# Kernel tuning notes

Hardware: AMD Instinct MI355X
Metric: run time of the kernel (lower is better)

Reference implementation:

```python
import jax, jax.numpy as jnp
import numpy as np

B, C, H, W = 4, 256, 64, 64
G, K, PAD, STRIDE, DIL, DWK = 8, 3, 1, 1, 1, 3
P = K * K
GC = C // G


def _dwconv(x, w, b, pad):
    # x: (B,C,H,W), w: (C,1,k,k) depthwise
    y = jax.lax.conv_general_dilated(x, w, (1, 1), [(pad, pad), (pad, pad)],
                                     feature_group_count=C,
                                     dimension_numbers=('NCHW', 'OIHW', 'NCHW'))
    return y + b[None, :, None, None]


def _conv1x1(x, w, b):
    # x: (B,Cin,H,W), w: (Cin,Cout)
    return jnp.einsum('bchw,cd->bdhw', x, w) + b[None, :, None, None]


def _ln(x, g, b, eps=1e-5):
    mu = x.mean(-1, keepdims=True)
    var = ((x - mu) ** 2).mean(-1, keepdims=True)
    return (x - mu) * jax.lax.rsqrt(var + eps) * g + b


def _bilinear_sample(img, grid):
    # img: (GC, Hp, Wp); grid: (L, P, 2) in [-1,1]; F.grid_sample bilinear,
    # padding_mode='zeros', align_corners=False
    gc, Hp, Wp = img.shape
    ix = ((grid[..., 0] + 1.0) * Wp - 1.0) * 0.5
    iy = ((grid[..., 1] + 1.0) * Hp - 1.0) * 0.5
    x0 = jnp.floor(ix); y0 = jnp.floor(iy)
    x1 = x0 + 1.0;      y1 = y0 + 1.0
    imgf = img.reshape(gc, Hp * Wp)

    def gather(yy, xx):
        valid = (xx >= 0) & (xx <= Wp - 1) & (yy >= 0) & (yy <= Hp - 1)
        xi = jnp.clip(xx, 0, Wp - 1).astype(jnp.int32)
        yi = jnp.clip(yy, 0, Hp - 1).astype(jnp.int32)
        return imgf[:, yi * Wp + xi] * valid  # (GC, L, P)

    w00 = (x1 - ix) * (y1 - iy); w01 = (ix - x0) * (y1 - iy)
    w10 = (x1 - ix) * (iy - y0); w11 = (ix - x0) * (iy - y0)
    return (gather(y0, x0) * w00 + gather(y0, x1) * w01 +
            gather(y1, x0) * w10 + gather(y1, x1) * w11)


def _dcnv3_core(x, offset, mask):
    # x: (B,H,W,C); offset: (B,H,W,G*P*2); mask: (B,H,W,G*P) softmaxed over P
    xp = jnp.pad(x, ((0, 0), (PAD, PAD), (PAD, PAD), (0, 0)))
    Hp, Wp = H + 2 * PAD, W + 2 * PAD
    base = (DIL * (K - 1)) // 2 + 0.5
    ref_y = (base + jnp.arange(H, dtype=jnp.float32) * STRIDE) / Hp
    ref_x = (base + jnp.arange(W, dtype=jnp.float32) * STRIDE) / Wp
    ref = jnp.stack([jnp.broadcast_to(ref_x[None, :], (H, W)),
                     jnp.broadcast_to(ref_y[:, None], (H, W))], -1)  # (H,W,2) (x,y)
    lin = jnp.arange(K, dtype=jnp.float32) * DIL - (DIL * (K - 1)) // 2
    gx, gy = jnp.meshgrid(lin, lin, indexing='ij')  # x-outer (torch meshgrid order)
    dil_grid = jnp.stack([gx / Wp, gy / Hp], -1).reshape(P, 2)
    loc = ref[:, :, None, None, :] + dil_grid[None, None, None, :, :]  # (H,W,1,P,2)
    loc = jnp.broadcast_to(loc, (H, W, G, P, 2))[None]
    norm = jnp.array([Wp, Hp], jnp.float32)
    loc = loc + offset.reshape(B, H, W, G, P, 2) / norm  # offset_scale=1.0
    sg = 2.0 * loc - 1.0  # (B,H,W,G,P,2)
    xin = xp.reshape(B, Hp, Wp, G, GC).transpose(0, 3, 4, 1, 2).reshape(B * G, GC, Hp, Wp)
    sgf = sg.reshape(B, H * W, G, P, 2).transpose(0, 2, 1, 3, 4).reshape(B * G, H * W, P, 2)
    sampled = jax.vmap(_bilinear_sample)(xin, sgf)  # (B*G, GC, HW, P)
    m = mask.reshape(B, H * W, G, P).transpose(0, 2, 1, 3).reshape(B * G, 1, H * W, P)
    out = (sampled * m).sum(-1)  # (B*G, GC, HW)
    return out.reshape(B, G, GC, H * W).transpose(0, 3, 1, 2).reshape(B, H, W, C)


def _dcn(x, inproj_w, inproj_b, dw_w, dw_b, ln_g, ln_b,
         off_w, off_b, mask_w, mask_b, outproj_w, outproj_b):
    # x: (B,H,W,C) -> DCNv3_pytorch forward
    xproj = x @ inproj_w + inproj_b
    x1 = _dwconv(x.transpose(0, 3, 1, 2), dw_w, dw_b, (DWK - 1) // 2).transpose(0, 2, 3, 1)
    x1 = jax.nn.gelu(_ln(x1, ln_g, ln_b), approximate=False)
    offset = x1 @ off_w + off_b
    m = jax.nn.softmax((x1 @ mask_w + mask_b).reshape(B, H, W, G, P), -1).reshape(B, H, W, G * P)
    out = _dcnv3_core(xproj, offset, m)
    return out @ outproj_w + outproj_b


def _forward(x, proj1_w, proj1_b, conv0_w, conv0_b, inproj_w, inproj_b,
             dw_w, dw_b, ln_g, ln_b, off_w, off_b, mask_w, mask_b,
             outproj_w, outproj_b, conv_w, conv_b, proj2_w, proj2_b):
    shortcut = x
    h = jax.nn.gelu(_conv1x1(x, proj1_w, proj1_b), approximate=False)
    u = h
    h = _dwconv(h, conv0_w, conv0_b, 2)  # 5x5 depthwise, pad 2
    attn = _dcn(h.transpose(0, 2, 3, 1), inproj_w, inproj_b, dw_w, dw_b,
                ln_g, ln_b, off_w, off_b, mask_w, mask_b, outproj_w, outproj_b)
    attn = _conv1x1(attn.transpose(0, 3, 1, 2), conv_w, conv_b)
    h = _conv1x1(u * attn, proj2_w, proj2_b)
    return h + shortcut


def setup_inputs():
    key = jax.random.key(0)
    ks = jax.random.split(key, 12)
    s = lambda k, shape, fan: jax.random.normal(k, shape, jnp.float32) / np.sqrt(fan)
    return {
        'x': jax.random.normal(ks[0], (B, C, H, W), jnp.float32),
        'proj1_w': s(ks[1], (C, C), C), 'proj1_b': jnp.zeros((C,), jnp.float32),
        'conv0_w': s(ks[2], (C, 1, 5, 5), 25), 'conv0_b': jnp.zeros((C,), jnp.float32),
        'inproj_w': s(ks[3], (C, C), C), 'inproj_b': jnp.zeros((C,), jnp.float32),
        'dw_w': s(ks[4], (C, 1, DWK, DWK), DWK * DWK), 'dw_b': jnp.zeros((C,), jnp.float32),
        'ln_g': jnp.ones((C,), jnp.float32), 'ln_b': jnp.zeros((C,), jnp.float32),
        'off_w': s(ks[5], (C, G * P * 2), C) * 0.1, 'off_b': jnp.zeros((G * P * 2,), jnp.float32),
        'mask_w': s(ks[6], (C, G * P), C), 'mask_b': jnp.zeros((G * P,), jnp.float32),
        'outproj_w': s(ks[7], (C, C), C), 'outproj_b': jnp.zeros((C,), jnp.float32),
        'conv_w': s(ks[8], (C, C), C), 'conv_b': jnp.zeros((C,), jnp.float32),
        'proj2_w': s(ks[9], (C, C), C), 'proj2_b': jnp.zeros((C,), jnp.float32),
    }


def reference(x, proj1_w, proj1_b, conv0_w, conv0_b, inproj_w, inproj_b,
              dw_w, dw_b, ln_g, ln_b, off_w, off_b, mask_w, mask_b,
              outproj_w, outproj_b, conv_w, conv_b, proj2_w, proj2_b):
    return _forward(x, proj1_w, proj1_b, conv0_w, conv0_b, inproj_w, inproj_b,
                    dw_w, dw_b, ln_g, ln_b, off_w, off_b, mask_w, mask_b,
                    outproj_w, outproj_b, conv_w, conv_b, proj2_w, proj2_b)
```

## Files before the change

kernel.cpp:

```cpp
#include <hip/hip_runtime.h>
#include <cstddef>

#define HW    4096
#define NPIX  16384
#define CCH   256

typedef __attribute__((ext_vector_type(8))) short bf16x8;
typedef __attribute__((ext_vector_type(4))) float f32x4;

__device__ __forceinline__ float gelu_f(float x){
    return 0.5f * x * (1.0f + erff(x * 0.70710678118654752f));
}

__device__ __forceinline__ unsigned short bf_rne(float f){
    unsigned u = __float_as_uint(f);
    u += 0x7FFFu + ((u >> 16) & 1u);
    return (unsigned short)(u >> 16);
}

__device__ __forceinline__ void split_cheap(const float4 a, const float4 b, bf16x8& hi, bf16x8& lo){
    const float v[8] = {a.x,a.y,a.z,a.w,b.x,b.y,b.z,b.w};
    #pragma unroll
    for (int j = 0; j < 8; j++){
        const unsigned u = __float_as_uint(v[j]);
        hi[j] = (short)(unsigned short)(u >> 16);
        const float r = v[j] - __uint_as_float(u & 0xFFFF0000u);
        lo[j] = (short)(unsigned short)(__float_as_uint(r) >> 16);
    }
}

__global__ __launch_bounds__(256) void k_prep(const float* __restrict__ w5,
                                              const float* __restrict__ w3,
                                              float* __restrict__ wT,
                                              float* __restrict__ wT3){
    const int c = threadIdx.x;
    const int j = blockIdx.x;
    wT[j * CCH + c] = w5[c * 25 + j];
    if (j < 9) wT3[j * CCH + c] = w3[c * 9 + j];
}

__global__ __launch_bounds__(256) void k_compose(const float* __restrict__ ow,
                                                 const float* __restrict__ cw,
                                                 const float* __restrict__ ob,
                                                 const float* __restrict__ cb,
                                                 float* __restrict__ woc,
                                                 float* __restrict__ boc){
    const int m = threadIdx.x;
    if (blockIdx.x == 256){
        float acc = cb[m];
        #pragma unroll 4
        for (int k = 0; k < 256; k++) acc = fmaf(ob[k], cw[k * 256 + m], acc);
        boc[m] = acc;
    } else {
        const int r = blockIdx.x;
        const float* orow = ow + r * 256;
        float acc = 0.f;
        #pragma unroll 4
        for (int k = 0; k < 256; k++) acc = fmaf(orow[k], cw[k * 256 + m], acc);
        woc[r * 256 + m] = acc;
    }
}

__global__ __launch_bounds__(256) void k_prep_w(
    const float* __restrict__ w0, const float* __restrict__ w1, const float* __restrict__ w2,
    const float* __restrict__ w3,
    const float* __restrict__ offw, const float* __restrict__ maskw,
    const float* __restrict__ offb, const float* __restrict__ maskb,
    unsigned short* __restrict__ wsp, float* __restrict__ bcat)
{
    __shared__ float tile[64][65];
    const int id = blockIdx.y;
    const int m0 = (blockIdx.x & 3) * 64;
    const int k0 = (blockIdx.x >> 2) * 64;
    const int tx = threadIdx.x & 63, tg = threadIdx.x >> 6;
    unsigned short* hi = wsp + (size_t)id * 131072;
    unsigned short* lo = hi + 65536;

    const int m = m0 + tx;
    const float* src = nullptr; int stride = 0; bool valid = true;
    if (id == 4){
        if (m < 144){ src = offw + m; stride = 144; }
        else if (m < 216){ src = maskw + (m - 144); stride = 72; }
        else valid = false;
    } else {
        const float* s = (id==0)?w0:(id==1)?w1:(id==2)?w2:w3;
        src = s + m; stride = 256;
    }
    #pragma unroll
    for (int i = 0; i < 16; i++){
        const int kl = tg * 16 + i;
        tile[kl][tx] = valid ? src[(size_t)(k0 + kl) * stride] : 0.f;
    }
    __syncthreads();
    #pragma unroll
    for (int i = 0; i < 16; i++){
        const int ml = tg * 16 + i;
        const float f = tile[tx][ml];
        const unsigned u = __float_as_uint(f);
        const size_t o = (size_t)(m0 + ml) * 256 + k0 + tx;
        hi[o] = (unsigned short)(u >> 16);
        lo[o] = bf_rne(f - __uint_as_float(u & 0xFFFF0000u));
    }
    if (id == 4 && blockIdx.x == 0){
        const int t = threadIdx.x;
        if (t < 216) bcat[t] = (t < 144) ? offb[t] : maskb[t - 144];
        else if (t < 224) bcat[t] = 0.f;
    }
}

__global__ __launch_bounds__(256) void k_transpose(const float* __restrict__ in,
                                                   float* __restrict__ out){
    __shared__ float tile[64][65];
    const int b = blockIdx.z, c0 = blockIdx.y * 64, hw0 = blockIdx.x * 64;
    const int tx = threadIdx.x & 63, tg = threadIdx.x >> 6;
    #pragma unroll
    for (int i = 0; i < 16; i++){
        const int c_l = tg * 16 + i;
        tile[c_l][tx] = in[(size_t)(b * CCH + c0 + c_l) * HW + hw0 + tx];
    }
    __syncthreads();
    #pragma unroll
    for (int i = 0; i < 16; i++){
        const int hw_l = tg * 16 + i;
        out[(size_t)(b * HW + hw0 + hw_l) * CCH + c0 + tx] = tile[tx][hw_l];
    }
}

template<int EPI, bool MUL>
__global__ __launch_bounds__(256) void k_gemm_bf(
    const float* __restrict__ A, const float* __restrict__ A2,
    const unsigned short* __restrict__ Whi, const unsigned short* __restrict__ Wlo,
    const float* __restrict__ bias, const float* __restrict__ resid,
    float* __restrict__ out, const int M, const int ldc)
{
    const int rows0 = blockIdx.x * 32;
    const int lane = threadIdx.x & 63;
    const int w    = threadIdx.x >> 6;
    const int wm = (w >> 1) * 16;
    const int wn = (w & 1) * 128;
    const int lr = lane & 15;
    const int kg = lane >> 4;
    const int kl = kg * 8;

    const float* Ap = A + (size_t)(rows0 + wm + lr) * 256 + kl;
    const float* Mp = MUL ? (A2 + (size_t)(rows0 + wm + lr) * 256 + kl) : nullptr;
    const int c0 = wn + lr;
    const unsigned short* Wh = Whi + (size_t)c0 * 256 + kl;
    const unsigned short* Wl = Wlo + (size_t)c0 * 256 + kl;

    const f32x4 z = {0.f, 0.f, 0.f, 0.f};
    f32x4 acc[8] = {z,z,z,z,z,z,z,z};

    #pragma unroll 2
    for (int kt = 0; kt < 8; kt++){
        const int k0 = kt * 32;
        float4 a0 = *reinterpret_cast<const float4*>(Ap + k0);
        float4 a1 = *reinterpret_cast<const float4*>(Ap + k0 + 4);
        if (MUL){
            const float4 u0 = *reinterpret_cast<const float4*>(Mp + k0);
            const float4 u1 = *reinterpret_cast<const float4*>(Mp + k0 + 4);
            a0.x*=u0.x; a0.y*=u0.y; a0.z*=u0.z; a0.w*=u0.w;
            a1.x*=u1.x; a1.y*=u1.y; a1.z*=u1.z; a1.w*=u1.w;
        }
        bf16x8 ah, al;
        split_cheap(a0, a1, ah, al);
        #pragma unroll
        for (int nf = 0; nf < 8; nf++){
            const size_t wo = (size_t)(nf * 16) * 256 + k0;
            const bf16x8 bh = *reinterpret_cast<const bf16x8*>(Wh + wo);
            const bf16x8 bl = *reinterpret_cast<const bf16x8*>(Wl + wo);
            acc[nf] = __builtin_amdgcn_mfma_f32_16x16x32_bf16(ah, bh, acc[nf], 0, 0, 0);
            acc[nf] = __builtin_amdgcn_mfma_f32_16x16x32_bf16(ah, bl, acc[nf], 0, 0, 0);
            acc[nf] = __builtin_amdgcn_mfma_f32_16x16x32_bf16(al, bh, acc[nf], 0, 0, 0);
        }
    }

    const int r4 = kg * 4;
    const int rowb = rows0 + wm + r4;
    if (EPI == 2){
        const int bimg = rowb >> 12;
        const int hw   = rowb & (HW - 1);
        #pragma unroll
        for (int nf = 0; nf < 8; nf++){
            const int col = c0 + nf * 16;
            const float bs = bias[col];
            const size_t addr = ((size_t)(bimg * CCH + col)) * HW + hw;
            const float4 rv = *reinterpret_cast<const float4*>(resid + addr);
            float4 o;
            o.x = acc[nf][0] + bs + rv.x;
            o.y = acc[nf][1] + bs + rv.y;
            o.z = acc[nf][2] + bs + rv.z;
            o.w = acc[nf][3] + bs + rv.w;
            *reinterpret_cast<float4*>(out + addr) = o;
        }
    } else {
        #pragma unroll
        for (int nf = 0; nf < 8; nf++){
            const int col = c0 + nf * 16;
            if (col < M){
                const float bs = bias[col];
                #pragma unroll
                for (int r = 0; r < 4; r++){
                    float v = acc[nf][r] + bs;
                    if (EPI == 1) v = gelu_f(v);
                    out[(size_t)(rowb + r) * ldc + col] = v;
                }
            }
        }
    }
}

__global__ __launch_bounds__(256) void k_dwconv5(const float* __restrict__ in,
                                                 const float* __restrict__ wT,
                                                 const float* __restrict__ bias,
                                                 float* __restrict__ out){
    const int lane = threadIdx.x & 63;
    const int pq   = threadIdx.x >> 6;
    const int n = blockIdx.x * 4 + pq;
    const int x = n & 63, y = (n >> 6) & 63, b = n >> 12;
    const int c = lane * 4;
    const float* bp = in + (size_t)(b * HW) * CCH + c;
    float4 acc = *reinterpret_cast<const float4*>(bias + c);
    #pragma unroll
    for (int k = 0; k < 25; k++){
        const int dy = k / 5 - 2, dx = k % 5 - 2;
        const int yy = y + dy, xx = x + dx;
        const float m = (((unsigned)yy < 64u) & ((unsigned)xx < 64u)) ? 1.f : 0.f;
        const int yc = min(max(yy, 0), 63), xc = min(max(xx, 0), 63);
        const float4 iv = *reinterpret_cast<const float4*>(bp + (size_t)(yc * 64 + xc) * CCH);
        const float4 wv = *reinterpret_cast<const float4*>(wT + k * CCH + c);
        acc.x = fmaf(iv.x, wv.x * m, acc.x);
        acc.y = fmaf(iv.y, wv.y * m, acc.y);
        acc.z = fmaf(iv.z, wv.z * m, acc.z);
        acc.w = fmaf(iv.w, wv.w * m, acc.w);
    }
    *reinterpret_cast<float4*>(out + (size_t)n * CCH + c) = acc;
}

__global__ __launch_bounds__(256) void k_dw3_ln_gelu(const float* __restrict__ in,
                                                     const float* __restrict__ wT3,
                                                     const float* __restrict__ b3,
                                                     const float* __restrict__ g,
                                                     const float* __restrict__ bta,
                                                     float* __restrict__ out){
    const int lane = threadIdx.x & 63;
    const int pq   = threadIdx.x >> 6;
    const int n = blockIdx.x * 4 + pq;
    const int x = n & 63, y = (n >> 6) & 63, b = n >> 12;
    const int c = lane * 4;
    const float* bp = in + (size_t)(b * HW) * CCH + c;
    float4 acc = *reinterpret_cast<const float4*>(b3 + c);
    #pragma unroll
    for (int k = 0; k < 9; k++){
        const int dy = k / 3 - 1, dx = k % 3 - 1;
        const int yy = y + dy, xx = x + dx;
        const float m = (((unsigned)yy < 64u) & ((unsigned)xx < 64u)) ? 1.f : 0.f;
        const int yc = min(max(yy, 0), 63), xc = min(max(xx, 0), 63);
        const float4 iv = *reinterpret_cast<const float4*>(bp + (size_t)(yc * 64 + xc) * CCH);
        const float4 wv = *reinterpret_cast<const float4*>(wT3 + k * CCH + c);
        acc.x = fmaf(iv.x, wv.x * m, acc.x);
        acc.y = fmaf(iv.y, wv.y * m, acc.y);
        acc.z = fmaf(iv.z, wv.z * m, acc.z);
        acc.w = fmaf(iv.w, wv.w * m, acc.w);
    }
    float s  = acc.x + acc.y + acc.z + acc.w;
    float s2 = acc.x*acc.x + acc.y*acc.y + acc.z*acc.z + acc.w*acc.w;
    #pragma unroll
    for (int o = 32; o > 0; o >>= 1){
        s  += __shfl_xor(s, o);
        s2 += __shfl_xor(s2, o);
    }
    const float mu  = s  * (1.f / 256.f);
    const float var = s2 * (1.f / 256.f) - mu * mu;
    const float r   = rsqrtf(var + 1e-5f);
    const float4 gv = *reinterpret_cast<const float4*>(g + c);
    const float4 bv = *reinterpret_cast<const float4*>(bta + c);
    float4 o;
    o.x = gelu_f((acc.x - mu) * r * gv.x + bv.x);
    o.y = gelu_f((acc.y - mu) * r * gv.y + bv.y);
    o.z = gelu_f((acc.z - mu) * r * gv.z + bv.z);
    o.w = gelu_f((acc.w - mu) * r * gv.w + bv.w);
    *reinterpret_cast<float4*>(out + (size_t)n * CCH + c) = o;
}

__global__ __launch_bounds__(256) void k_dcn(const float* __restrict__ xproj,
                                             const float* __restrict__ om,
                                             float* __restrict__ out){
    const int lane = threadIdx.x & 63;
    const int pq   = threadIdx.x >> 6;
    const int n = blockIdx.x * 4 + pq;
    const int gI = lane >> 3, cq = lane & 7;
    const int x = n & 63, y = (n >> 6) & 63, b = n >> 12;
    const float* off = om + (size_t)n * 216 + gI * 18;
    const float* lg  = om + (size_t)n * 216 + 144 + gI * 9;
    float l[9]; float mx = -1e30f;
    #pragma unroll
    for (int p = 0; p < 9; p++){ l[p] = lg[p]; mx = fmaxf(mx, l[p]); }
    float ssum = 0.f;
    #pragma unroll
    for (int p = 0; p < 9; p++){ l[p] = expf(l[p] - mx); ssum += l[p]; }
    const float inv = 1.f / ssum;
    const float* base = xproj + (size_t)b * HW * CCH + gI * 32 + cq * 4;
    float4 acc = {0.f, 0.f, 0.f, 0.f};
    #pragma unroll
    for (int p = 0; p < 9; p++){
        const float2 o2 = *reinterpret_cast<const float2*>(off + p * 2);
        const float ix = (float)(x + p / 3) + o2.x;
        const float iy = (float)(y + p % 3) + o2.y;
        const float x0f = floorf(ix), y0f = floorf(iy);
        const float wx1 = ix - x0f, wy1 = iy - y0f;
        const float wx0 = 1.f - wx1, wy0 = 1.f - wy1;
        const int ux = (int)x0f - 1, uy = (int)y0f - 1;
        const bool X0 = (unsigned)ux     < 64u, X1 = (unsigned)(ux+1) < 64u;
        const bool Y0 = (unsigned)uy     < 64u, Y1 = (unsigned)(uy+1) < 64u;
        const int ux0 = min(max(ux,     0), 63), ux1 = min(max(ux + 1, 0), 63);
        const int uy0 = min(max(uy,     0), 63), uy1 = min(max(uy + 1, 0), 63);
        const float mp = l[p] * inv;
        const float w00 = wx0 * wy0 * ((X0 & Y0) ? mp : 0.f);
        const float w01 = wx1 * wy0 * ((X1 & Y0) ? mp : 0.f);
        const float w10 = wx0 * wy1 * ((X0 & Y1) ? mp : 0.f);
        const float w11 = wx1 * wy1 * ((X1 & Y1) ? mp : 0.f);
        const float4 v00 = *reinterpret_cast<const float4*>(base + (size_t)(uy0 * 64 + ux0) * CCH);
        const float4 v01 = *reinterpret_cast<const float4*>(base + (size_t)(uy0 * 64 + ux1) * CCH);
        const float4 v10 = *reinterpret_cast<const float4*>(base + (size_t)(uy1 * 64 + ux0) * CCH);
        const float4 v11 = *reinterpret_cast<const float4*>(base + (size_t)(uy1 * 64 + ux1) * CCH);
        acc.x = fmaf(w00, v00.x, fmaf(w01, v01.x, fmaf(w10, v10.x, fmaf(w11, v11.x, acc.x))));
        acc.y = fmaf(w00, v00.y, fmaf(w01, v01.y, fmaf(w10, v10.y, fmaf(w11, v11.y, acc.y))));
        acc.z = fmaf(w00, v00.z, fmaf(w01, v01.z, fmaf(w10, v10.z, fmaf(w11, v11.z, acc.z))));
        acc.w = fmaf(w00, v00.w, fmaf(w01, v01.w, fmaf(w10, v10.w, fmaf(w11, v11.w, acc.w))));
    }
    *reinterpret_cast<float4*>(out + (size_t)n * CCH + gI * 32 + cq * 4) = acc;
}

extern "C" void kernel_launch(void* const* d_in, const int* in_sizes, int n_in,
                              void* d_out, int out_size, void* d_ws, size_t ws_size,
                              hipStream_t stream){
    const float* x         = (const float*)d_in[0];
    const float* proj1_w   = (const float*)d_in[1];
    const float* proj1_b   = (const float*)d_in[2];
    const float* conv0_w   = (const float*)d_in[3];
    const float* conv0_b   = (const float*)d_in[4];
    const float* inproj_w  = (const float*)d_in[5];
    const float* inproj_b  = (const float*)d_in[6];
    const float* dw_w      = (const float*)d_in[7];
    const float* dw_b      = (const float*)d_in[8];
    const float* ln_g      = (const float*)d_in[9];
    const float* ln_b      = (const float*)d_in[10];
    const float* off_w     = (const float*)d_in[11];
    const float* off_b     = (const float*)d_in[12];
    const float* mask_w    = (const float*)d_in[13];
    const float* mask_b    = (const float*)d_in[14];
    const float* outproj_w = (const float*)d_in[15];
    const float* outproj_b = (const float*)d_in[16];
    const float* conv_w    = (const float*)d_in[17];
    const float* conv_b    = (const float*)d_in[18];
    const float* proj2_w   = (const float*)d_in[19];
    const float* proj2_b   = (const float*)d_in[20];
    float* outp = (float*)d_out;

    const size_t NC = (size_t)NPIX * CCH;
    float* b0 = (float*)d_ws;
    float* b1 = b0 + NC;
    float* b2 = b1 + NC;
    float* b3 = outp;
    unsigned short* wsp = (unsigned short*)(b2 + NC);
    float* bcat = (float*)(wsp + 5 * 131072);
    float* woc  = bcat + 224;
    float* boc  = woc + 65536;
    float* wT   = b3;
    float* wT3  = b3 + 25 * CCH;

    const unsigned short* whi[5]; const unsigned short* wlo[5];
    for (int i = 0; i < 5; i++){ whi[i] = wsp + (size_t)i * 131072; wlo[i] = whi[i] + 65536; }

    k_prep<<<25,256,0,stream>>>(conv0_w, dw_w, wT, wT3);
    k_compose<<<257,256,0,stream>>>(outproj_w, conv_w, outproj_b, conv_b, woc, boc);
    k_prep_w<<<dim3(16,5),256,0,stream>>>(proj1_w, inproj_w, woc, proj2_w,
                                          off_w, mask_w, off_b, mask_b, wsp, bcat);
    k_transpose<<<dim3(64,4,4),256,0,stream>>>(x, b0);
    k_gemm_bf<1,false><<<512,256,0,stream>>>(b0, nullptr, whi[0], wlo[0], proj1_b, nullptr, b1, 256, 256);
    k_dwconv5<<<4096,256,0,stream>>>(b1, wT, conv0_b, b2);
    k_dw3_ln_gelu<<<4096,256,0,stream>>>(b2, wT3, dw_b, ln_g, ln_b, b0);
    k_gemm_bf<0,false><<<512,256,0,stream>>>(b2, nullptr, whi[1], wlo[1], inproj_b, nullptr, b3, 256, 256);
    k_gemm_bf<0,false><<<512,256,0,stream>>>(b0, nullptr, whi[4], wlo[4], bcat, nullptr, b2, 216, 216);
    k_dcn<<<4096,256,0,stream>>>(b3, b2, b0);
    k_gemm_bf<0,false><<<512,256,0,stream>>>(b0, nullptr, whi[2], wlo[2], boc, nullptr, b2, 256, 256);
    k_gemm_bf<2,true><<<512,256,0,stream>>>(b1, b2, whi[3], wlo[3], proj2_b, x, outp, 256, 256);
}
```

Baseline: 391.5 us.

## Retile bf16x3 GEMM to 64x128 blocks with 2D grid and vectorized epilogue

Changes the split-bf16 GEMM tiling from 32 rows by 256 columns per block to 64 rows by 128 columns, using a 2D grid so each wave computes a 32x64 tile that reuses each weight fragment across two row fragments. For the non-residual epilogues, MFMA operands are swapped so each lane holds four consecutive output columns, which allows float4 bias loads and float4 stores instead of scalar strided stores. The low-part split now uses round-to-nearest instead of truncation, trading a few extra ALU ops for accuracy.

```diff
diff --git a/kernel.cpp b/kernel.cpp
--- a/kernel.cpp
+++ b/kernel.cpp
@@ -18,14 +18,13 @@
     return (unsigned short)(u >> 16);
 }
 
-__device__ __forceinline__ void split_cheap(const float4 a, const float4 b, bf16x8& hi, bf16x8& lo){
+__device__ __forceinline__ void split2(const float4 a, const float4 b, bf16x8& hi, bf16x8& lo){
     const float v[8] = {a.x,a.y,a.z,a.w,b.x,b.y,b.z,b.w};
     #pragma unroll
     for (int j = 0; j < 8; j++){
         const unsigned u = __float_as_uint(v[j]);
         hi[j] = (short)(unsigned short)(u >> 16);
-        const float r = v[j] - __uint_as_float(u & 0xFFFF0000u);
-        lo[j] = (short)(unsigned short)(__float_as_uint(r) >> 16);
+        lo[j] = (short)bf_rne(v[j] - __uint_as_float(u & 0xFFFF0000u));
     }
 }
 
@@ -133,77 +132,106 @@
     const float* __restrict__ bias, const float* __restrict__ resid,
     float* __restrict__ out, const int M, const int ldc)
 {
-    const int rows0 = blockIdx.x * 32;
+    const int rows0 = blockIdx.x * 64;
+    const int cols0 = blockIdx.y * 128;
     const int lane = threadIdx.x & 63;
     const int w    = threadIdx.x >> 6;
-    const int wm = (w >> 1) * 16;
-    const int wn = (w & 1) * 128;
+    const int wm = (w >> 1) * 32, wn = (w & 1) * 64;
     const int lr = lane & 15;
     const int kg = lane >> 4;
     const int kl = kg * 8;
 
-    const float* Ap = A + (size_t)(rows0 + wm + lr) * 256 + kl;
-    const float* Mp = MUL ? (A2 + (size_t)(rows0 + wm + lr) * 256 + kl) : nullptr;
-    const int c0 = wn + lr;
-    const unsigned short* Wh = Whi + (size_t)c0 * 256 + kl;
-    const unsigned short* Wl = Wlo + (size_t)c0 * 256 + kl;
+    const float* Ap0 = A + (size_t)(rows0 + wm + lr) * 256 + kl;
+    const float* Ap1 = Ap0 + 16 * 256;
+    const float* Mp0 = MUL ? (A2 + (size_t)(rows0 + wm + lr) * 256 + kl) : nullptr;
+    const float* Mp1 = MUL ? (Mp0 + 16 * 256) : nullptr;
+    const int cw = cols0 + wn + lr;
+    const unsigned short* Wh = Whi + (size_t)cw * 256 + kl;
+    const unsigned short* Wl = Wlo + (size_t)cw * 256 + kl;
 
     const f32x4 z = {0.f, 0.f, 0.f, 0.f};
-    f32x4 acc[8] = {z,z,z,z,z,z,z,z};
+    f32x4 acc[2][4] = {{z,z,z,z},{z,z,z,z}};
 
     #pragma unroll 2
     for (int kt = 0; kt < 8; kt++){
         const int k0 = kt * 32;
-        float4 a0 = *reinterpret_cast<const float4*>(Ap + k0);
-        float4 a1 = *reinterpret_cast<const float4*>(Ap + k0 + 4);
+        float4 a0 = *reinterpret_cast<const float4*>(Ap0 + k0);
+        float4 a1 = *reinterpret_cast<const float4*>(Ap0 + k0 + 4);
+        float4 a2 = *reinterpret_cast<const float4*>(Ap1 + k0);
+        float4 a3 = *reinterpret_cast<const float4*>(Ap1 + k0 + 4);
         if (MUL){
-            const float4 u0 = *reinterpret_cast<const float4*>(Mp + k0);
-            const float4 u1 = *reinterpret_cast<const float4*>(Mp + k0 + 4);
+            const float4 u0 = *reinterpret_cast<const float4*>(Mp0 + k0);
+            const float4 u1 = *reinterpret_cast<const float4*>(Mp0 + k0 + 4);
+            const float4 u2 = *reinterpret_cast<const float4*>(Mp1 + k0);
+            const float4 u3 = *reinterpret_cast<const float4*>(Mp1 + k0 + 4);
             a0.x*=u0.x; a0.y*=u0.y; a0.z*=u0.z; a0.w*=u0.w;
             a1.x*=u1.x; a1.y*=u1.y; a1.z*=u1.z; a1.w*=u1.w;
+            a2.x*=u2.x; a2.y*=u2.y; a2.z*=u2.z; a2.w*=u2.w;
+            a3.x*=u3.x; a3.y*=u3.y; a3.z*=u3.z; a3.w*=u3.w;
         }
-        bf16x8 ah, al;
-        split_cheap(a0, a1, ah, al);
+        bf16x8 ah0, al0, ah1, al1;
+        split2(a0, a1, ah0, al0);
+        split2(a2, a3, ah1, al1);
         #pragma unroll
-        for (int nf = 0; nf < 8; nf++){
-            const size_t wo = (size_t)(nf * 16) * 256 + k0;
+        for (int c = 0; c < 4; c++){
+            const size_t wo = (size_t)(c * 16) * 256 + k0;
             const bf16x8 bh = *reinterpret_cast<const bf16x8*>(Wh + wo);
             const bf16x8 bl = *reinterpret_cast<const bf16x8*>(Wl + wo);
-            acc[nf] = __builtin_amdgcn_mfma_f32_16x16x32_bf16(ah, bh, acc[nf], 0, 0, 0);
-            acc[nf] = __builtin_amdgcn_mfma_f32_16x16x32_bf16(ah, bl, acc[nf], 0, 0, 0);
-            acc[nf] = __builtin_amdgcn_mfma_f32_16x16x32_bf16(al, bh, acc[nf], 0, 0, 0);
+            if (EPI == 2){
+                acc[0][c] = __builtin_amdgcn_mfma_f32_16x16x32_bf16(ah0, bh, acc[0][c], 0, 0, 0);
+                acc[0][c] = __builtin_amdgcn_mfma_f32_16x16x32_bf16(ah0, bl, acc[0][c], 0, 0, 0);
+                acc[0][c] = __builtin_amdgcn_mfma_f32_16x16x32_bf16(al0, bh, acc[0][c], 0, 0, 0);
+                acc[1][c] = __builtin_amdgcn_mfma_f32_16x16x32_bf16(ah1, bh, acc[1][c], 0, 0, 0);
+                acc[1][c] = __builtin_amdgcn_mfma_f32_16x16x32_bf16(ah1, bl, acc[1][c], 0, 0, 0);
+                acc[1][c] = __builtin_amdgcn_mfma_f32_16x16x32_bf16(al1, bh, acc[1][c], 0, 0, 0);
+            } else {
+                acc[0][c] = __builtin_amdgcn_mfma_f32_16x16x32_bf16(bh, ah0, acc[0][c], 0, 0, 0);
+                acc[0][c] = __builtin_amdgcn_mfma_f32_16x16x32_bf16(bh, al0, acc[0][c], 0, 0, 0);
+                acc[0][c] = __builtin_amdgcn_mfma_f32_16x16x32_bf16(bl, ah0, acc[0][c], 0, 0, 0);
+                acc[1][c] = __builtin_amdgcn_mfma_f32_16x16x32_bf16(bh, ah1, acc[1][c], 0, 0, 0);
+                acc[1][c] = __builtin_amdgcn_mfma_f32_16x16x32_bf16(bh, al1, acc[1][c], 0, 0, 0);
+                acc[1][c] = __builtin_amdgcn_mfma_f32_16x16x32_bf16(bl, ah1, acc[1][c], 0, 0, 0);
+            }
         }
     }
 
     const int r4 = kg * 4;
-    const int rowb = rows0 + wm + r4;
     if (EPI == 2){
-        const int bimg = rowb >> 12;
-        const int hw   = rowb & (HW - 1);
         #pragma unroll
-        for (int nf = 0; nf < 8; nf++){
-            const int col = c0 + nf * 16;
-            const float bs = bias[col];
-            const size_t addr = ((size_t)(bimg * CCH + col)) * HW + hw;
-            const float4 rv = *reinterpret_cast<const float4*>(resid + addr);
-            float4 o;
-            o.x = acc[nf][0] + bs + rv.x;
-            o.y = acc[nf][1] + bs + rv.y;
-            o.z = acc[nf][2] + bs + rv.z;
-            o.w = acc[nf][3] + bs + rv.w;
-            *reinterpret_cast<float4*>(out + addr) = o;
+        for (int f = 0; f < 2; f++){
+            const int n = rows0 + wm + f * 16 + r4;
+            const int bimg = n >> 12;
+            const int hw = n & (HW - 1);
+            #pragma unroll
+            for (int c = 0; c < 4; c++){
+                const int col = cw + c * 16;
+                const float bs = bias[col];
+                const size_t addr = ((size_t)(bimg * CCH + col)) * HW + hw;
+                const float4 rv = *reinterpret_cast<const float4*>(resid + addr);
+                float4 o;
+                o.x = acc[f][c][0] + bs + rv.x;
+                o.y = acc[f][c][1] + bs + rv.y;
+                o.z = acc[f][c][2] + bs + rv.z;
+                o.w = acc[f][c][3] + bs + rv.w;
+                *reinterpret_cast<float4*>(out + addr) = o;
+            }
         }
     } else {
         #pragma unroll
-        for (int nf = 0; nf < 8; nf++){
-            const int col = c0 + nf * 16;
-            if (col < M){
-                const float bs = bias[col];
-                #pragma unroll
-                for (int r = 0; r < 4; r++){
-                    float v = acc[nf][r] + bs;
-                    if (EPI == 1) v = gelu_f(v);
-                    out[(size_t)(rowb + r) * ldc + col] = v;
+        for (int f = 0; f < 2; f++){
+            const int n = rows0 + wm + f * 16 + lr;
+            #pragma unroll
+            for (int c = 0; c < 4; c++){
+                const int mb = cols0 + wn + c * 16 + r4;
+                if (mb < M){
+                    const float4 bv = *reinterpret_cast<const float4*>(bias + mb);
+                    float4 o;
+                    o.x = acc[f][c][0] + bv.x;
+                    o.y = acc[f][c][1] + bv.y;
+                    o.z = acc[f][c][2] + bv.z;
+                    o.w = acc[f][c][3] + bv.w;
+                    if (EPI == 1){ o.x=gelu_f(o.x); o.y=gelu_f(o.y); o.z=gelu_f(o.z); o.w=gelu_f(o.w); }
+                    *reinterpret_cast<float4*>(out + (size_t)n * ldc + mb) = o;
                 }
             }
         }
@@ -373,17 +401,19 @@
     const unsigned short* whi[5]; const unsigned short* wlo[5];
     for (int i = 0; i < 5; i++){ whi[i] = wsp + (size_t)i * 131072; wlo[i] = whi[i] + 65536; }
 
+    const dim3 G(256, 2);
+
     k_prep<<<25,256,0,stream>>>(conv0_w, dw_w, wT, wT3);
     k_compose<<<257,256,0,stream>>>(outproj_w, conv_w, outproj_b, conv_b, woc, boc);
     k_prep_w<<<dim3(16,5),256,0,stream>>>(proj1_w, inproj_w, woc, proj2_w,
                                           off_w, mask_w, off_b, mask_b, wsp, bcat);
     k_transpose<<<dim3(64,4,4),256,0,stream>>>(x, b0);
-    k_gemm_bf<1,false><<<512,256,0,stream>>>(b0, nullptr, whi[0], wlo[0], proj1_b, nullptr, b1, 256, 256);
+    k_gemm_bf<1,false><<<G,256,0,stream>>>(b0, nullptr, whi[0], wlo[0], proj1_b, nullptr, b1, 256, 256);
     k_dwconv5<<<4096,256,0,stream>>>(b1, wT, conv0_b, b2);
     k_dw3_ln_gelu<<<4096,256,0,stream>>>(b2, wT3, dw_b, ln_g, ln_b, b0);
-    k_gemm_bf<0,false><<<512,256,0,stream>>>(b2, nullptr, whi[1], wlo[1], inproj_b, nullptr, b3, 256, 256);
-    k_gemm_bf<0,false><<<512,256,0,stream>>>(b0, nullptr, whi[4], wlo[4], bcat, nullptr, b2, 216, 216);
+    k_gemm_bf<0,false><<<G,256,0,stream>>>(b2, nullptr, whi[1], wlo[1], inproj_b, nullptr, b3, 256, 256);
+    k_gemm_bf<0,false><<<G,256,0,stream>>>(b0, nullptr, whi[4], wlo[4], bcat, nullptr, b2, 216, 216);
     k_dcn<<<4096,256,0,stream>>>(b3, b2, b0);
-    k_gemm_bf<0,false><<<512,256,0,stream>>>(b0, nullptr, whi[2], wlo[2], boc, nullptr, b2, 256, 256);
-    k_gemm_bf<2,true><<<512,256,0,stream>>>(b1, b2, whi[3], wlo[3], proj2_b, x, outp, 256, 256);
-}
+    k_gemm_bf<0,false><<<G,256,0,stream>>>(b0, nullptr, whi[2], wlo[2], boc, nullptr, b2, 256, 256);
+    k_gemm_bf<2,true><<<G,256,0,stream>>>(b1, b2, whi[3], wlo[3], proj2_b, x, outp, 256, 256);
+}
```

Measured after the change: 346.7 us. 11.4% less time.

## Shrink GEMM tiles to 16x128 over a 2D grid with swapped MFMA operands

Applied to the files above, without the earlier changes.

The bf16-split GEMM now uses 16-row by 128-column blocks on a 1024x2 grid instead of 32x256 blocks, which cuts each wave's accumulators from eight to two and raises occupancy (launch bounds 256,8). For non-residual epilogues the MFMA operands are swapped so each lane holds four consecutive output columns, enabling float4 bias loads and float4 stores. The low half of the split is now round-to-nearest rather than truncated. Weights are loaded more often per output row because each block reuses them across fewer rows.

```diff
diff --git a/kernel.cpp b/kernel.cpp
--- a/kernel.cpp
+++ b/kernel.cpp
@@ -18,14 +18,13 @@
     return (unsigned short)(u >> 16);
 }
 
-__device__ __forceinline__ void split_cheap(const float4 a, const float4 b, bf16x8& hi, bf16x8& lo){
+__device__ __forceinline__ void split2(const float4 a, const float4 b, bf16x8& hi, bf16x8& lo){
     const float v[8] = {a.x,a.y,a.z,a.w,b.x,b.y,b.z,b.w};
     #pragma unroll
     for (int j = 0; j < 8; j++){
         const unsigned u = __float_as_uint(v[j]);
         hi[j] = (short)(unsigned short)(u >> 16);
-        const float r = v[j] - __uint_as_float(u & 0xFFFF0000u);
-        lo[j] = (short)(unsigned short)(__float_as_uint(r) >> 16);
+        lo[j] = (short)bf_rne(v[j] - __uint_as_float(u & 0xFFFF0000u));
     }
 }
 
@@ -127,29 +126,29 @@
 }
 
 template<int EPI, bool MUL>
-__global__ __launch_bounds__(256) void k_gemm_bf(
+__global__ __launch_bounds__(256, 8) void k_gemm_bf(
     const float* __restrict__ A, const float* __restrict__ A2,
     const unsigned short* __restrict__ Whi, const unsigned short* __restrict__ Wlo,
     const float* __restrict__ bias, const float* __restrict__ resid,
     float* __restrict__ out, const int M, const int ldc)
 {
-    const int rows0 = blockIdx.x * 32;
+    const int rows0 = blockIdx.x * 16;
+    const int cols0 = blockIdx.y * 128;
     const int lane = threadIdx.x & 63;
     const int w    = threadIdx.x >> 6;
-    const int wm = (w >> 1) * 16;
-    const int wn = (w & 1) * 128;
+    const int wn   = w * 32;
     const int lr = lane & 15;
     const int kg = lane >> 4;
     const int kl = kg * 8;
 
-    const float* Ap = A + (size_t)(rows0 + wm + lr) * 256 + kl;
-    const float* Mp = MUL ? (A2 + (size_t)(rows0 + wm + lr) * 256 + kl) : nullptr;
-    const int c0 = wn + lr;
-    const unsigned short* Wh = Whi + (size_t)c0 * 256 + kl;
-    const unsigned short* Wl = Wlo + (size_t)c0 * 256 + kl;
+    const float* Ap = A + (size_t)(rows0 + lr) * 256 + kl;
+    const float* Mp = MUL ? (A2 + (size_t)(rows0 + lr) * 256 + kl) : nullptr;
+    const int cw0 = cols0 + wn + lr;
+    const unsigned short* Wh = Whi + (size_t)cw0 * 256 + kl;
+    const unsigned short* Wl = Wlo + (size_t)cw0 * 256 + kl;
 
     const f32x4 z = {0.f, 0.f, 0.f, 0.f};
-    f32x4 acc[8] = {z,z,z,z,z,z,z,z};
+    f32x4 acc[2] = {z, z};
 
     #pragma unroll 2
     for (int kt = 0; kt < 8; kt++){
@@ -163,48 +162,56 @@
             a1.x*=u1.x; a1.y*=u1.y; a1.z*=u1.z; a1.w*=u1.w;
         }
         bf16x8 ah, al;
-        split_cheap(a0, a1, ah, al);
+        split2(a0, a1, ah, al);
         #pragma unroll
-        for (int nf = 0; nf < 8; nf++){
-            const size_t wo = (size_t)(nf * 16) * 256 + k0;
+        for (int c = 0; c < 2; c++){
+            const size_t wo = (size_t)(c * 16) * 256 + k0;
             const bf16x8 bh = *reinterpret_cast<const bf16x8*>(Wh + wo);
             const bf16x8 bl = *reinterpret_cast<const bf16x8*>(Wl + wo);
-            acc[nf] = __builtin_amdgcn_mfma_f32_16x16x32_bf16(ah, bh, acc[nf], 0, 0, 0);
-            acc[nf] = __builtin_amdgcn_mfma_f32_16x16x32_bf16(ah, bl, acc[nf], 0, 0, 0);
-            acc[nf] = __builtin_amdgcn_mfma_f32_16x16x32_bf16(al, bh, acc[nf], 0, 0, 0);
+            if (EPI == 2){
+                acc[c] = __builtin_amdgcn_mfma_f32_16x16x32_bf16(ah, bh, acc[c], 0, 0, 0);
+                acc[c] = __builtin_amdgcn_mfma_f32_16x16x32_bf16(ah, bl, acc[c], 0, 0, 0);
+                acc[c] = __builtin_amdgcn_mfma_f32_16x16x32_bf16(al, bh, acc[c], 0, 0, 0);
+            } else {
+                acc[c] = __builtin_amdgcn_mfma_f32_16x16x32_bf16(bh, ah, acc[c], 0, 0, 0);
+                acc[c] = __builtin_amdgcn_mfma_f32_16x16x32_bf16(bh, al, acc[c], 0, 0, 0);
+                acc[c] = __builtin_amdgcn_mfma_f32_16x16x32_bf16(bl, ah, acc[c], 0, 0, 0);
+            }
         }
     }
 
     const int r4 = kg * 4;
-    const int rowb = rows0 + wm + r4;
     if (EPI == 2){
-        const int bimg = rowb >> 12;
-        const int hw   = rowb & (HW - 1);
+        const int n = rows0 + r4;
+        const int bimg = n >> 12;
+        const int hw   = n & (HW - 1);
         #pragma unroll
-        for (int nf = 0; nf < 8; nf++){
-            const int col = c0 + nf * 16;
+        for (int c = 0; c < 2; c++){
+            const int col = cw0 + c * 16;
             const float bs = bias[col];
             const size_t addr = ((size_t)(bimg * CCH + col)) * HW + hw;
             const float4 rv = *reinterpret_cast<const float4*>(resid + addr);
             float4 o;
-            o.x = acc[nf][0] + bs + rv.x;
-            o.y = acc[nf][1] + bs + rv.y;
-            o.z = acc[nf][2] + bs + rv.z;
-            o.w = acc[nf][3] + bs + rv.w;
+            o.x = acc[c][0] + bs + rv.x;
+            o.y = acc[c][1] + bs + rv.y;
+            o.z = acc[c][2] + bs + rv.z;
+            o.w = acc[c][3] + bs + rv.w;
             *reinterpret_cast<float4*>(out + addr) = o;
         }
     } else {
+        const int n = rows0 + lr;
         #pragma unroll
-        for (int nf = 0; nf < 8; nf++){
-            const int col = c0 + nf * 16;
-            if (col < M){
-                const float bs = bias[col];
-                #pragma unroll
-                for (int r = 0; r < 4; r++){
-                    float v = acc[nf][r] + bs;
-                    if (EPI == 1) v = gelu_f(v);
-                    out[(size_t)(rowb + r) * ldc + col] = v;
-                }
+        for (int c = 0; c < 2; c++){
+            const int mb = cols0 + wn + c * 16 + r4;
+            if (mb < M){
+                const float4 bv = *reinterpret_cast<const float4*>(bias + mb);
+                float4 o;
+                o.x = acc[c][0] + bv.x;
+                o.y = acc[c][1] + bv.y;
+                o.z = acc[c][2] + bv.z;
+                o.w = acc[c][3] + bv.w;
+                if (EPI == 1){ o.x=gelu_f(o.x); o.y=gelu_f(o.y); o.z=gelu_f(o.z); o.w=gelu_f(o.w); }
+                *reinterpret_cast<float4*>(out + (size_t)n * ldc + mb) = o;
             }
         }
     }
@@ -373,17 +380,19 @@
     const unsigned short* whi[5]; const unsigned short* wlo[5];
     for (int i = 0; i < 5; i++){ whi[i] = wsp + (size_t)i * 131072; wlo[i] = whi[i] + 65536; }
 
+    const dim3 G(1024, 2);
+
     k_prep<<<25,256,0,stream>>>(conv0_w, dw_w, wT, wT3);
     k_compose<<<257,256,0,stream>>>(outproj_w, conv_w, outproj_b, conv_b, woc, boc);
     k_prep_w<<<dim3(16,5),256,0,stream>>>(proj1_w, inproj_w, woc, proj2_w,
                                           off_w, mask_w, off_b, mask_b, wsp, bcat);
     k_transpose<<<dim3(64,4,4),256,0,stream>>>(x, b0);
-    k_gemm_bf<1,false><<<512,256,0,stream>>>(b0, nullptr, whi[0], wlo[0], proj1_b, nullptr, b1, 256, 256);
+    k_gemm_bf<1,false><<<G,256,0,stream>>>(b0, nullptr, whi[0], wlo[0], proj1_b, nullptr, b1, 256, 256);
     k_dwconv5<<<4096,256,0,stream>>>(b1, wT, conv0_b, b2);
     k_dw3_ln_gelu<<<4096,256,0,stream>>>(b2, wT3, dw_b, ln_g, ln_b, b0);
-    k_gemm_bf<0,false><<<512,256,0,stream>>>(b2, nullptr, whi[1], wlo[1], inproj_b, nullptr, b3, 256, 256);
-    k_gemm_bf<0,false><<<512,256,0,stream>>>(b0, nullptr, whi[4], wlo[4], bcat, nullptr, b2, 216, 216);
+    k_gemm_bf<0,false><<<G,256,0,stream>>>(b2, nullptr, whi[1], wlo[1], inproj_b, nullptr, b3, 256, 256);
+    k_gemm_bf<0,false><<<G,256,0,stream>>>(b0, nullptr, whi[4], wlo[4], bcat, nullptr, b2, 216, 216);
     k_dcn<<<4096,256,0,stream>>>(b3, b2, b0);
-    k_gemm_bf<0,false><<<512,256,0,stream>>>(b0, nullptr, whi[2], wlo[2], boc, nullptr, b2, 256, 256);
-    k_gemm_bf<2,true><<<512,256,0,stream>>>(b1, b2, whi[3], wlo[3], proj2_b, x, outp, 256, 256);
-}
+    k_gemm_bf<0,false><<<G,256,0,stream>>>(b0, nullptr, whi[2], wlo[2], boc, nullptr, b2, 256, 256);
+    k_gemm_bf<2,true><<<G,256,0,stream>>>(b1, b2, whi[3], wlo[3], proj2_b, x, outp, 256, 256);
+}
```

After: 442.6 us. +13.1%, slower.
